# Kernel tuning notes

Hardware: AMD Instinct MI355X
Metric: run time of the kernel (lower is better)

## Reference

```python
import jax, jax.numpy as jnp
import numpy as np

N, DIM, H, DH = 2048, 1024, 16, 64
LARGE_NEG = -1e10
LN_EPS = 1e-6  # flax LayerNorm default


def setup_inputs() -> dict:
    key = jax.random.key(0)
    ks = jax.random.split(key, 6)
    x = jax.random.normal(ks[0], (N, DIM), dtype=jnp.float32)
    pos_sin = jax.random.uniform(ks[1], (N - 1, DH // 2), dtype=jnp.float32)
    pos_cos = jax.random.uniform(ks[2], (N - 1, DH // 2), dtype=jnp.float32)
    mask = jax.random.bernoulli(ks[3], 0.9, (N - 1,))
    ln_scale = jnp.ones((DIM,), jnp.float32)
    ln_bias = jnp.zeros((DIM,), jnp.float32)
    w_qkv = jax.random.normal(ks[4], (DIM, 3 * H * DH), jnp.float32) * (DIM ** -0.5)
    w_out = jax.random.normal(ks[5], (H * DH, DIM), jnp.float32) * ((H * DH) ** -0.5)
    b_out = jnp.zeros((DIM,), jnp.float32)
    return {"x": x, "pos_sin": pos_sin, "pos_cos": pos_cos, "mask": mask,
            "ln_scale": ln_scale, "ln_bias": ln_bias,
            "w_qkv": w_qkv, "w_out": w_out, "b_out": b_out}


def _rotate_every_two(t):
    # t: [i, h, d] -> pairwise rotation along d
    x1 = t[:, :, ::2]
    x2 = t[:, :, 1::2]
    return jnp.stack((-x2, x1), axis=-1).reshape(t.shape)


def _apply_rope(t, sin, cos):
    # sin/cos: [i, d/2] -> interleave-repeat to [i, 1, d] (einops 'b n -> b (n j)', j=2)
    sin2 = jnp.repeat(sin, 2, axis=-1)[:, None, :]
    cos2 = jnp.repeat(cos, 2, axis=-1)[:, None, :]
    return t * cos2 + _rotate_every_two(t) * sin2


def reference(x, pos_sin, pos_cos, mask, ln_scale, ln_bias, w_qkv, w_out, b_out):
    n, dim_in = x.shape
    scale = dim_in ** -0.5  # NOTE: full model dim, as in the source

    # LayerNorm over last axis
    mu = jnp.mean(x, axis=-1, keepdims=True)
    var = jnp.mean(jnp.square(x - mu), axis=-1, keepdims=True)
    xn = (x - mu) * jax.lax.rsqrt(var + LN_EPS) * ln_scale + ln_bias

    # QKV projection (no bias)
    qkv = xn @ w_qkv  # [n, 3*h*d]
    q, k, v = jnp.split(qkv, 3, axis=-1)
    q, k, v = (t.reshape(n, H, DH) for t in (q, k, v))

    # Selective RoPE: rotate all positions except the first token
    q = q.at[1:].set(_apply_rope(q[1:], pos_sin, pos_cos))
    k = k.at[1:].set(_apply_rope(k[1:], pos_sin, pos_cos))

    # Head-last similarity [i, j, h]
    sim = jnp.einsum('ihd,jhd->ijh', q, k) * scale

    # Padding mask: prepend True for position 0, broadcast as (1, j, 1)
    pad_mask = jnp.pad(mask, (1, 0), constant_values=True)[None, :, None]

    # Causal mask: triu of an (n-1)x(n-1) block padded with False on row/col 0
    tri = jnp.pad(jnp.ones((n - 1, n - 1), bool), ((1, 0), (1, 0)), constant_values=False)
    causal_mask = jnp.triu(tri, 1)[:, :, None]  # k = j - i + 1 = 1
    full_mask = (~causal_mask) & pad_mask

    sim = jnp.where(full_mask, sim, LARGE_NEG)
    attn = jax.nn.softmax(sim, axis=-2)  # softmax over j (non-last axis)

    out = jnp.einsum('ijh,jhd->ihd', attn, v).reshape(n, H * DH)
    return out @ w_out + b_out
```

## Files before the change

kernel.cpp:

```cpp
#include <hip/hip_runtime.h>
#include <hip/hip_bf16.h>
#include <stdint.h>

typedef __bf16 bf16_t;
typedef __bf16 bf16x8 __attribute__((ext_vector_type(8)));
typedef __bf16 bf16x4 __attribute__((ext_vector_type(4)));
typedef float  f32x4  __attribute__((ext_vector_type(4)));

#define DEV __device__ __forceinline__

static constexpr int NTOK = 2048;
static constexpr int DIM  = 1024;
static constexpr int NH   = 16;
static constexpr int DH   = 64;
static constexpr int SLOTS_PER_HEAD = 40;
static constexpr int PART_SLOTS = 36;
static constexpr int PART_STRIDE = 17408;
static constexpr float L2E = 1.44269504f;

__device__ static constexpr unsigned char SLOT_ORDER[40] = {
    39, 38, 37, 36, 34, 33, 32, 30, 29, 28, 26, 25, 24, 23,
    22, 21, 19, 18, 16, 15, 13, 12, 11, 10, 8, 6, 4, 3,
    35, 20, 9, 2,
    31, 17, 7, 1,
    27, 14, 5, 0};

DEV void gload_lds16(const void* g, void* l) {
  __builtin_amdgcn_global_load_lds(
      (__attribute__((address_space(1))) void*)(g),
      (__attribute__((address_space(3))) void*)(l), 16, 0, 0);
}

DEV float bf2f(bf16_t b) { return (float)b; }

__global__ __launch_bounds__(256) void k_ln_tc(const float* __restrict__ x,
                                               const float* __restrict__ gamma,
                                               const float* __restrict__ beta,
                                               bf16_t* __restrict__ xn,
                                               const float* __restrict__ wsrc,
                                               bf16_t* __restrict__ wdst,
                                               const float* __restrict__ wosrc,
                                               bf16_t* __restrict__ wodst) {
  __shared__ float tile[64][65];
  __shared__ float red[8];
  int b = blockIdx.x;
  if (b < NTOK) {
    const int row = b;
    const int t = threadIdx.x;
    const float4* x4 = reinterpret_cast<const float4*>(x);
    float4 v = x4[(size_t)row * 256 + t];
    float s  = v.x + v.y + v.z + v.w;
    float s2 = v.x * v.x + v.y * v.y + v.z * v.z + v.w * v.w;
#pragma unroll
    for (int o = 1; o < 64; o <<= 1) {
      s  += __shfl_xor(s, o, 64);
      s2 += __shfl_xor(s2, o, 64);
    }
    const int w = t >> 6, lane = t & 63;
    if (lane == 0) { red[w] = s; red[4 + w] = s2; }
    __syncthreads();
    s  = red[0] + red[1] + red[2] + red[3];
    s2 = red[4] + red[5] + red[6] + red[7];
    const float mu  = s * (1.0f / 1024.0f);
    const float var = s2 * (1.0f / 1024.0f) - mu * mu;
    const float inv = rsqrtf(var + 1e-6f);
    const float4 g = reinterpret_cast<const float4*>(gamma)[t];
    const float4 bb = reinterpret_cast<const float4*>(beta)[t];
    bf16x4 o;
    o[0] = (bf16_t)((v.x - mu) * inv * g.x + bb.x);
    o[1] = (bf16_t)((v.y - mu) * inv * g.y + bb.y);
    o[2] = (bf16_t)((v.z - mu) * inv * g.z + bb.z);
    o[3] = (bf16_t)((v.w - mu) * inv * g.w + bb.w);
    *reinterpret_cast<bf16x4*>(xn + (size_t)row * DIM + t * 4) = o;
  } else if (b < NTOK + 768) {
    b -= NTOK;
    const int c0 = (b % 48) * 64;
    const int r0 = (b / 48) * 64;
    const int tx = threadIdx.x & 63;
    const int ty = threadIdx.x >> 6;
#pragma unroll
    for (int i = 0; i < 16; ++i) {
      int r = ty + i * 4;
      tile[r][tx] = wsrc[(size_t)(r0 + r) * 3072 + c0 + tx];
    }
    __syncthreads();
#pragma unroll
    for (int i = 0; i < 16; ++i) {
      int r = ty + i * 4;
      wdst[(size_t)(c0 + r) * 1024 + r0 + tx] = (bf16_t)tile[tx][r];
    }
  } else {
    b -= (NTOK + 768);
    const int c0 = (b & 15) * 64;
    const int r0 = (b >> 4) * 64;
    const int tx = threadIdx.x & 63;
    const int ty = threadIdx.x >> 6;
#pragma unroll
    for (int i = 0; i < 16; ++i) {
      int r = ty + i * 4;
      tile[r][tx] = wosrc[(size_t)(r0 + r) * 1024 + c0 + tx];
    }
    __syncthreads();
#pragma unroll
    for (int i = 0; i < 16; ++i) {
      int r = ty + i * 4;
      wodst[(size_t)(c0 + r) * 1024 + r0 + tx] = (bf16_t)tile[tx][r];
    }
  }
}

__global__ __launch_bounds__(256) void k_gemm_qkv(const bf16_t* __restrict__ A,
                                                  const bf16_t* __restrict__ Bt,
                                                  bf16_t* __restrict__ Qp,
                                                  bf16_t* __restrict__ Kp,
                                                  bf16_t* __restrict__ Vt,
                                                  const float* __restrict__ psin,
                                                  const float* __restrict__ pcos) {
  __shared__ alignas(16) bf16_t As[2][128 * 32];
  __shared__ alignas(16) bf16_t Bs[2][128 * 32];
  const int K = DIM;
  const int tid = threadIdx.x, lane = tid & 63, w = tid >> 6;
  const int bm = blockIdx.x * 128, bn = blockIdx.y * 128;
  const int wr = (w >> 1) * 64, wc = (w & 1) * 64;
  f32x4 acc[4][4];
#pragma unroll
  for (int i = 0; i < 4; ++i)
#pragma unroll
    for (int j = 0; j < 4; ++j) acc[i][j] = f32x4{0.f, 0.f, 0.f, 0.f};

  const int srow  = lane >> 2;
  const int scol8 = (lane & 3) * 8;

#define GSTAGEQ(KT, BUF)                                                              \
  {                                                                                   \
    _Pragma("unroll") for (int it = 0; it < 2; ++it) {                                \
      int seg = w * 2 + it;                                                           \
      gload_lds16(A  + (size_t)(bm + seg * 16 + srow) * K + (KT) + scol8,             \
                  (char*)As + (BUF) * 8192 + seg * 1024 + lane * 16);                 \
      gload_lds16(Bt + (size_t)(bn + seg * 16 + srow) * K + (KT) + scol8,             \
                  (char*)Bs + (BUF) * 8192 + seg * 1024 + lane * 16);                 \
    }                                                                                 \
  }

  GSTAGEQ(0, 0)
  int buf = 0;
  for (int kt = 0; kt < K; kt += 32, buf ^= 1) {
    if (kt + 32 < K) {
      GSTAGEQ(kt + 32, buf ^ 1)
      asm volatile("s_waitcnt vmcnt(4)" ::: "memory");
    } else {
      asm volatile("s_waitcnt vmcnt(0)" ::: "memory");
    }
    __builtin_amdgcn_s_barrier();
    bf16x8 af[4], bfr[4];
#pragma unroll
    for (int i = 0; i < 4; ++i) {
      int mrow = wr + i * 16 + (lane & 15);
      af[i] = *reinterpret_cast<const bf16x8*>((const char*)As + buf * 8192 + mrow * 64 +
                                               (lane >> 4) * 16);
    }
#pragma unroll
    for (int j = 0; j < 4; ++j) {
      int nrow = wc + j * 16 + (lane & 15);
      bfr[j] = *reinterpret_cast<const bf16x8*>((const char*)Bs + buf * 8192 + nrow * 64 +
                                                (lane >> 4) * 16);
    }
#pragma unroll
    for (int i = 0; i < 4; ++i)
#pragma unroll
      for (int j = 0; j < 4; ++j)
        acc[i][j] = __builtin_amdgcn_mfma_f32_16x16x32_bf16(af[i], bfr[j], acc[i][j], 0, 0, 0);
    __builtin_amdgcn_s_barrier();
  }
#undef GSTAGEQ

  if (bn >= 2048) {
#pragma unroll
    for (int i = 0; i < 4; ++i)
#pragma unroll
      for (int j = 0; j < 4; ++j) {
        int d = bn - 2048 + wc + j * 16 + (lane & 15);
        int n0v = bm + wr + i * 16 + (lane >> 4) * 4;
        bf16x4 v4;
#pragma unroll
        for (int r = 0; r < 4; ++r) v4[r] = (bf16_t)acc[i][j][r];
        *reinterpret_cast<bf16x4*>(Vt + (size_t)d * NTOK + n0v) = v4;
      }
  } else {
#pragma unroll
    for (int i = 0; i < 4; ++i)
#pragma unroll
      for (int j = 0; j < 4; ++j) {
        int nn = bn + wc + j * 16 + (lane & 15);
        int tt = (nn & 63) >> 1;
        bool isq = nn < 1024;
#pragma unroll
        for (int r = 0; r < 4; ++r) {
          int mm = bm + wr + i * 16 + (lane >> 4) * 4 + r;
          float v = acc[i][j][r];
          float p = __shfl_xor(v, 1, 64);
          int pidx = (mm >= 1 ? mm - 1 : 0) * 32 + tt;
          float sn = psin[pidx], cs = pcos[pidx];
          float roped = (nn & 1) ? (v * cs + p * sn) : (v * cs - p * sn);
          if (mm < 1) roped = v;
          if (isq && mm >= 1) roped *= 0.03125f;
          if (isq)
            Qp[(size_t)mm * DIM + nn] = (bf16_t)roped;
          else {
            int hh = (nn - 1024) >> 6, dd = nn & 63;
            Kp[((size_t)hh * NTOK + mm) * DH + dd] = (bf16_t)roped;
          }
        }
      }
  }
}

__global__ __launch_bounds__(256) void k_gemm64(const bf16_t* __restrict__ A,
                                                const bf16_t* __restrict__ Bt,
                                                float* __restrict__ Cf,
                                                const float* __restrict__ bias,
                                                int M, int N, int K) {
  __shared__ alignas(16) bf16_t As[2][64 * 32];
  __shared__ alignas(16) bf16_t Bs[2][64 * 32];
  const int tid = threadIdx.x, lane = tid & 63, w = tid >> 6;
  const int bm = blockIdx.x * 64, bn = blockIdx.y * 64;
  const int wr = (w >> 1) * 32, wc = (w & 1) * 32;
  f32x4 acc[2][2];
#pragma unroll
  for (int i = 0; i < 2; ++i)
#pragma unroll
    for (int j = 0; j < 2; ++j) acc[i][j] = f32x4{0.f, 0.f, 0.f, 0.f};

  const int srow  = lane >> 2;
  const int scol8 = (lane & 3) * 8;

#define GSTAGE64(KT, BUF)                                                             \
  {                                                                                   \
    _Pragma("unroll") for (int it = 0; it < 2; ++it) {                                \
      int s = w * 2 + it;                                                             \
      if (s < 4)                                                                      \
        gload_lds16(A + (size_t)(bm + s * 16 + srow) * K + (KT) + scol8,              \
                    (char*)As + (BUF) * 4096 + s * 1024 + lane * 16);                 \
      else                                                                            \
        gload_lds16(Bt + (size_t)(bn + (s - 4) * 16 + srow) * K + (KT) + scol8,       \
                    (char*)Bs + (BUF) * 4096 + (s - 4) * 1024 + lane * 16);           \
    }                                                                                 \
  }

  GSTAGE64(0, 0)
  int buf = 0;
  for (int kt = 0; kt < K; kt += 32, buf ^= 1) {
    if (kt + 32 < K) {
      GSTAGE64(kt + 32, buf ^ 1)
      asm volatile("s_waitcnt vmcnt(2)" ::: "memory");
    } else {
      asm volatile("s_waitcnt vmcnt(0)" ::: "memory");
    }
    __builtin_amdgcn_s_barrier();
    bf16x8 af[2], bfr[2];
#pragma unroll
    for (int i = 0; i < 2; ++i) {
      int mrow = wr + i * 16 + (lane & 15);
      af[i] = *reinterpret_cast<const bf16x8*>((const char*)As + buf * 4096 + mrow * 64 +
                                               (lane >> 4) * 16);
    }
#pragma unroll
    for (int j = 0; j < 2; ++j) {
      int nrow = wc + j * 16 + (lane & 15);
      bfr[j] = *reinterpret_cast<const bf16x8*>((const char*)Bs + buf * 4096 + nrow * 64 +
                                                (lane >> 4) * 16);
    }
#pragma unroll
    for (int i = 0; i < 2; ++i)
#pragma unroll
      for (int j = 0; j < 2; ++j)
        acc[i][j] = __builtin_amdgcn_mfma_f32_16x16x32_bf16(af[i], bfr[j], acc[i][j], 0, 0, 0);
    __builtin_amdgcn_s_barrier();
  }
#undef GSTAGE64

#pragma unroll
  for (int i = 0; i < 2; ++i)
#pragma unroll
    for (int j = 0; j < 2; ++j)
#pragma unroll
      for (int r = 0; r < 4; ++r) {
        int mm = bm + wr + i * 16 + (lane >> 4) * 4 + r;
        int nn = bn + wc + j * 16 + (lane & 15);
        Cf[(size_t)mm * N + nn] = acc[i][j][r] + bias[nn];
      }
}

__global__ __launch_bounds__(512) void k_attn_part(const bf16_t* __restrict__ Qp,
                                                   const bf16_t* __restrict__ Kp,
                                                   const bf16_t* __restrict__ Vt,
                                                   const int* __restrict__ mask,
                                                   char* __restrict__ part,
                                                   bf16_t* __restrict__ Ob) {
  __shared__ alignas(16) bf16_t Ks[2][64][64];
  __shared__ alignas(16) bf16_t Vs[2][64][64];
  __shared__ alignas(16) float padf[512];

  const int idx = blockIdx.x;
  const int h = idx & 15;
  const int rank = idx >> 4;

  if (rank == 0) {
    float* qv   = padf;
    float* sbuf = (float*)Ks;
    float* red  = (float*)Vs;
    float* red2 = (float*)Vs + 64;
    const int t = threadIdx.x, lane = t & 63, w8 = t >> 6;
    if (t < 64) qv[t] = (float)Qp[h * DH + t];
    __syncthreads();
    float sm[4];
    float lmax = -1e30f;
#pragma unroll
    for (int p = 0; p < 4; ++p) {
      int j = p * 512 + t;
      const bf16_t* kr = Kp + ((size_t)h * NTOK + j) * DH;
      float s = 0.f;
#pragma unroll
      for (int u = 0; u < 8; ++u) {
        bf16x8 kv8 = *reinterpret_cast<const bf16x8*>(kr + u * 8);
#pragma unroll
        for (int e = 0; e < 8; ++e) s += qv[u * 8 + e] * (float)kv8[e];
      }
      bool padj = (j == 0) || (mask[j - 1] != 0);
      s = padj ? s * 0.03125f : -1e30f;
      sm[p] = s;
      lmax = fmaxf(lmax, s);
    }
#pragma unroll
    for (int o = 1; o < 64; o <<= 1) lmax = fmaxf(lmax, __shfl_xor(lmax, o, 64));
    if (lane == 0) red[w8] = lmax;
    __syncthreads();
    float M = red[0];
#pragma unroll
    for (int i = 1; i < 8; ++i) M = fmaxf(M, red[i]);
    __syncthreads();
    float ls = 0.f;
#pragma unroll
    for (int p = 0; p < 4; ++p) {
      float pe = __expf(sm[p] - M);
      sbuf[p * 512 + t] = pe;
      ls += pe;
    }
#pragma unroll
    for (int o = 1; o < 64; o <<= 1) ls += __shfl_xor(ls, o, 64);
    if (lane == 0) red[w8] = ls;
    __syncthreads();
    float L = red[0];
#pragma unroll
    for (int i = 1; i < 8; ++i) L += red[i];

    const int d = t & 63, qr = t >> 6;
    const bf16_t* vr = Vt + ((size_t)h * DH + d) * NTOK + qr * 256;
    float a = 0.f;
#pragma unroll 8
    for (int u = 0; u < 32; ++u) {
      bf16x8 v8 = *reinterpret_cast<const bf16x8*>(vr + u * 8);
#pragma unroll
      for (int e = 0; e < 8; ++e) a += sbuf[qr * 256 + u * 8 + e] * (float)v8[e];
    }
    red2[qr * 64 + d] = a;
    __syncthreads();
    if (t < 64) {
      float o = 0.f;
#pragma unroll
      for (int i = 0; i < 8; ++i) o += red2[i * 64 + t];
      Ob[h * DH + t] = (bf16_t)(o / L);
    }
    return;
  }

  const int slot = SLOT_ORDER[rank - 1];
  int gq;
  if (slot < 4) gq = 0; else if (slot < 12) gq = 1; else if (slot < 24) gq = 2; else gq = 3;
  const int tt = slot - 2 * gq * (gq + 1);
  const int Q = (gq << 2) + tt / (gq + 1);
  const int c2 = tt - (tt / (gq + 1)) * (gq + 1);
  const int q0 = Q * 128;
  const int kbeg = c2 * 512;
  const int kvlen = (Q + 1) * 128;
  const int klen = min(512, kvlen - kbeg);
  const int ntiles = klen >> 6;
  const int nch = gq + 1;

  const int tid = threadIdx.x, lane = tid & 63, w = tid >> 6;
  const int g = lane >> 4;
  const int c = lane & 15;

  for (int jr = tid; jr < klen; jr += 512) {
    int j = kbeg + jr;
    padf[jr] = (j == 0 || mask[j - 1] != 0) ? 1.f : 0.f;
  }

  const int iw = q0 + w * 16;
  bf16x8 qf[2];
  {
    const bf16_t* qp = Qp + (size_t)(iw + c) * DIM + h * DH + g * 8;
    qf[0] = *reinterpret_cast<const bf16x8*>(qp);
    qf[1] = *reinterpret_cast<const bf16x8*>(qp + 32);
  }
  bf16x8 ones;
#pragma unroll
  for (int e = 0; e < 8; ++e) ones[e] = (bf16_t)1.0f;

  float m_run = -1e30f, m2 = -1e30f;
  f32x4 acc[4], accl;
#pragma unroll
  for (int df = 0; df < 4; ++df) acc[df] = f32x4{0.f, 0.f, 0.f, 0.f};
  accl = f32x4{0.f, 0.f, 0.f, 0.f};

  const int r8 = lane >> 3;

#define STAGE(KB, BUF)                                                                   \
  {                                                                                      \
    _Pragma("unroll") for (int i2 = 0; i2 < 2; ++i2) {                                   \
      int s = w * 2 + i2;                                                                \
      int sw = (lane & 7) ^ r8 ^ ((s & 3) << 1);                                         \
      if (s < 8) {                                                                       \
        int row = s * 8 + r8;                                                            \
        gload_lds16(Kp + ((size_t)h * NTOK + (KB) + row) * DH + sw * 8,                  \
                    (char*)Ks + (BUF)*8192 + s * 1024 + lane * 16);                      \
      } else {                                                                           \
        int row = (s - 8) * 8 + r8;                                                      \
        gload_lds16(Vt + ((size_t)h * DH + row) * NTOK + (KB) + sw * 8,                  \
                    (char*)Vs + (BUF)*8192 + (s - 8) * 1024 + lane * 16);                \
      }                                                                                  \
    }                                                                                    \
  }

  STAGE(kbeg, 0)

  for (int it = 0; it < ntiles; ++it) {
    const int buf = it & 1;
    if (it + 1 < ntiles) {
      STAGE(kbeg + (it + 1) * 64, buf ^ 1)
      asm volatile("s_waitcnt vmcnt(2)" ::: "memory");
    } else {
      asm volatile("s_waitcnt vmcnt(0)" ::: "memory");
    }
    __builtin_amdgcn_s_barrier();

    const int k0 = kbeg + it * 64;
    if (k0 <= iw + 15) {
      const char* KsT = (const char*)Ks + buf * 8192;
      const char* VsT = (const char*)Vs + buf * 8192;

      f32x4 sfr[4];
      __builtin_amdgcn_s_setprio(1);
#pragma unroll
      for (int f = 0; f < 4; ++f) {
        int key7 = ((f & 1) * 4) | (c & 3);
        int key = (f >> 1) * 32 + (c >> 2) * 8 + key7;
        int phi = key7 ^ (((c >> 2) & 3) << 1);
        f32x4 s = f32x4{0.f, 0.f, 0.f, 0.f};
#pragma unroll
        for (int kd = 0; kd < 2; ++kd) {
          bf16x8 kf = *reinterpret_cast<const bf16x8*>(
              KsT + key * 128 + (((kd * 4 + g) ^ phi) << 4));
          s = __builtin_amdgcn_mfma_f32_16x16x32_bf16(kf, qf[kd], s, 0, 0, 0);
        }
        sfr[f] = s;
      }
      __builtin_amdgcn_s_setprio(0);

      float pm = fmaxf(fmaxf(sfr[0][0], sfr[0][1]), fmaxf(sfr[0][2], sfr[0][3]));
#pragma unroll
      for (int f = 1; f < 4; ++f)
        pm = fmaxf(pm, fmaxf(fmaxf(sfr[f][0], sfr[f][1]), fmaxf(sfr[f][2], sfr[f][3])));
      pm = fmaxf(pm, __shfl_xor(pm, 16, 64));
      pm = fmaxf(pm, __shfl_xor(pm, 32, 64));

      if (!__all(pm <= m_run + 8.f)) {
        float mnew = fmaxf(m_run, pm);
        float corr = __builtin_amdgcn_exp2f((m_run - mnew) * L2E);
        m_run = mnew;
        m2 = mnew * L2E;
#pragma unroll
        for (int r = 0; r < 4; ++r) {
          float cr = __shfl(corr, g * 4 + r, 64);
          accl[r] *= cr;
#pragma unroll
          for (int df = 0; df < 4; ++df) acc[df][r] *= cr;
        }
      }

      const bool needC = (k0 + 63 > iw);
      const int qlane = iw + c;
      bf16x8 pa[2];
#pragma unroll
      for (int f = 0; f < 4; ++f) {
        int jb = (k0 - kbeg) + (f >> 1) * 32 + g * 8 + (f & 1) * 4;
        f32x4 pad4 = *reinterpret_cast<const f32x4*>(padf + jb);
#pragma unroll
        for (int r = 0; r < 4; ++r) {
          float pe = __builtin_amdgcn_exp2f(__builtin_fmaf(sfr[f][r], L2E, -m2)) * pad4[r];
          if (needC) pe = (kbeg + jb + r <= qlane) ? pe : 0.f;
          pa[f >> 1][(f & 1) * 4 + r] = (bf16_t)pe;
        }
      }

      __builtin_amdgcn_s_setprio(1);
#pragma unroll
      for (int ks = 0; ks < 2; ++ks) {
        accl = __builtin_amdgcn_mfma_f32_16x16x32_bf16(pa[ks], ones, accl, 0, 0, 0);
#pragma unroll
        for (int df = 0; df < 4; ++df) {
          int d = df * 16 + c;
          int phv = (d & 7) ^ (((d >> 3) & 3) << 1);
          bf16x8 vf = *reinterpret_cast<const bf16x8*>(
              VsT + d * 128 + (((ks * 4 + g) ^ phv) << 4));
          acc[df] = __builtin_amdgcn_mfma_f32_16x16x32_bf16(pa[ks], vf, acc[df], 0, 0, 0);
        }
      }
      __builtin_amdgcn_s_setprio(0);
    }
    __builtin_amdgcn_s_barrier();
  }
#undef STAGE

  if (nch == 1) {
#pragma unroll
    for (int r = 0; r < 4; ++r) {
      float inv = 1.0f / accl[r];
      int row = w * 16 + g * 4 + r;
#pragma unroll
      for (int df = 0; df < 4; ++df) {
        if (q0 + row != 0)
          Ob[(size_t)(q0 + row) * DIM + h * DH + df * 16 + c] = (bf16_t)(acc[df][r] * inv);
      }
    }
    return;
  }

  char* pb = part + (size_t)(h * PART_SLOTS + (slot - 4)) * PART_STRIDE;
  bf16_t* po = (bf16_t*)pb;
  float* pmo = (float*)(pb + 16384);
  float* plo = (float*)(pb + 16896);
  float mq[4];
#pragma unroll
  for (int r = 0; r < 4; ++r) mq[r] = __shfl(m2, g * 4 + r, 64);
#pragma unroll
  for (int df = 0; df < 4; ++df)
#pragma unroll
    for (int r = 0; r < 4; ++r) {
      int row = w * 16 + g * 4 + r;
      po[row * 64 + df * 16 + c] = (bf16_t)acc[df][r];
    }
  if (c == 0) {
#pragma unroll
    for (int r = 0; r < 4; ++r) {
      int row = w * 16 + g * 4 + r;
      pmo[row] = mq[r];
      plo[row] = accl[r];
    }
  }
}

__global__ __launch_bounds__(256) void k_merge(const char* __restrict__ part,
                                               bf16_t* __restrict__ Ob) {
  const int Q = blockIdx.x + 4, h = blockIdx.y;
  const int g = Q >> 2, nch = g + 1;
  const int cum = 2 * g * (g + 1) + (Q & 3) * nch - 4;
  const int t = threadIdx.x;
  const int row = t >> 1, half = t & 1;

  float acc[32];
#pragma unroll
  for (int e = 0; e < 32; ++e) acc[e] = 0.f;
  float M = -3e38f, L = 0.f;

  for (int c = 0; c < nch; ++c) {
    const char* pb = part + (size_t)(h * PART_SLOTS + cum + c) * PART_STRIDE;
    float mc = ((const float*)(pb + 16384))[row];
    float lc = ((const float*)(pb + 16896))[row];
    float Mn = fmaxf(M, mc);
    float sOld = __builtin_amdgcn_exp2f(M - Mn), sNew = __builtin_amdgcn_exp2f(mc - Mn);
    M = Mn;
    L = L * sOld + lc * sNew;
    const bf16_t* od = (const bf16_t*)pb + row * 64 + half * 32;
#pragma unroll
    for (int e4 = 0; e4 < 4; ++e4) {
      bf16x8 o8 = *reinterpret_cast<const bf16x8*>(od + e4 * 8);
#pragma unroll
      for (int e = 0; e < 8; ++e)
        acc[e4 * 8 + e] = acc[e4 * 8 + e] * sOld + (float)o8[e] * sNew;
    }
  }
  const float inv = 1.0f / L;
  bf16_t* dst = Ob + (size_t)(Q * 128 + row) * DIM + h * DH + half * 32;
#pragma unroll
  for (int e4 = 0; e4 < 4; ++e4) {
    bf16x8 r8o;
#pragma unroll
    for (int e = 0; e < 8; ++e) r8o[e] = (bf16_t)(acc[e4 * 8 + e] * inv);
    *reinterpret_cast<bf16x8*>(dst + e4 * 8) = r8o;
  }
}

extern "C" void kernel_launch(void* const* d_in, const int* in_sizes, int n_in,
                              void* d_out, int out_size, void* d_ws, size_t ws_size,
                              hipStream_t stream) {
  const float* x       = (const float*)d_in[0];
  const float* pos_sin = (const float*)d_in[1];
  const float* pos_cos = (const float*)d_in[2];
  const int*   mask    = (const int*)d_in[3];
  const float* ln_s    = (const float*)d_in[4];
  const float* ln_b    = (const float*)d_in[5];
  const float* w_qkv   = (const float*)d_in[6];
  const float* w_out   = (const float*)d_in[7];
  const float* b_out   = (const float*)d_in[8];
  float* out = (float*)d_out;

  if (ws_size < 33554432u) return;

  char* ws = (char*)d_ws;
  bf16_t* Qp   = (bf16_t*)(ws + 0);
  bf16_t* Kp   = (bf16_t*)(ws + 4194304);
  bf16_t* Vt   = (bf16_t*)(ws + 8388608);
  bf16_t* Ob   = (bf16_t*)(ws + 12582912);
  bf16_t* Wot  = (bf16_t*)(ws + 16777216);
  bf16_t* xn   = (bf16_t*)(ws + 18874368);
  bf16_t* Wqt  = (bf16_t*)(ws + 23068672);
  char*   part = ws + 18874368;

  k_ln_tc<<<NTOK + 768 + 256, 256, 0, stream>>>(x, ln_s, ln_b, xn, w_qkv, Wqt, w_out, Wot);
  k_gemm_qkv<<<dim3(16, 24), 256, 0, stream>>>(xn, Wqt, Qp, Kp, Vt, pos_sin, pos_cos);
  k_attn_part<<<16 * (SLOTS_PER_HEAD + 1), 512, 0, stream>>>(Qp, Kp, Vt, mask, part, Ob);
  k_merge<<<dim3(12, 16), 256, 0, stream>>>(part, Ob);
  k_gemm64<<<dim3(32, 16), 256, 0, stream>>>(Ob, Wot, out, b_out, NTOK, DIM, DIM);
}
```

Measured before the change: 86.33 us.

## Fuse split-KV merge into attention kernel via last-block atomic counter

Removes the separate merge kernel launch. Each attention partial block atomically increments a per-(head, query-block) counter after writing its partial output, and the last block to arrive combines all partials and writes the normalized result. The counters are zeroed by an extra block in the layernorm/transpose kernel and stored in the output buffer, which the final GEMM later overwrites. This saves a launch and the gap between kernels, at the cost of threadfences, an atomic per block and a serialized merge tail in whichever block finishes last.

```diff
diff --git a/kernel.cpp b/kernel.cpp
--- a/kernel.cpp
+++ b/kernel.cpp
@@ -40,7 +40,8 @@
                                                const float* __restrict__ wsrc,
                                                bf16_t* __restrict__ wdst,
                                                const float* __restrict__ wosrc,
-                                               bf16_t* __restrict__ wodst) {
+                                               bf16_t* __restrict__ wodst,
+                                               int* __restrict__ cnt) {
   __shared__ float tile[64][65];
   __shared__ float red[8];
   int b = blockIdx.x;
@@ -89,7 +90,7 @@
       int r = ty + i * 4;
       wdst[(size_t)(c0 + r) * 1024 + r0 + tx] = (bf16_t)tile[tx][r];
     }
-  } else {
+  } else if (b < NTOK + 768 + 256) {
     b -= (NTOK + 768);
     const int c0 = (b & 15) * 64;
     const int r0 = (b >> 4) * 64;
@@ -106,6 +107,8 @@
       int r = ty + i * 4;
       wodst[(size_t)(c0 + r) * 1024 + r0 + tx] = (bf16_t)tile[tx][r];
     }
+  } else {
+    cnt[threadIdx.x] = 0;
   }
 }
 
@@ -296,10 +299,12 @@
                                                    const bf16_t* __restrict__ Vt,
                                                    const int* __restrict__ mask,
                                                    char* __restrict__ part,
-                                                   bf16_t* __restrict__ Ob) {
+                                                   bf16_t* __restrict__ Ob,
+                                                   int* __restrict__ cnt) {
   __shared__ alignas(16) bf16_t Ks[2][64][64];
   __shared__ alignas(16) bf16_t Vs[2][64][64];
   __shared__ alignas(16) float padf[512];
+  __shared__ int isLast;
 
   const int idx = blockIdx.x;
   const int h = idx & 15;
@@ -537,67 +542,71 @@
   }
 
   char* pb = part + (size_t)(h * PART_SLOTS + (slot - 4)) * PART_STRIDE;
-  bf16_t* po = (bf16_t*)pb;
-  float* pmo = (float*)(pb + 16384);
-  float* plo = (float*)(pb + 16896);
-  float mq[4];
-#pragma unroll
-  for (int r = 0; r < 4; ++r) mq[r] = __shfl(m2, g * 4 + r, 64);
-#pragma unroll
-  for (int df = 0; df < 4; ++df)
-#pragma unroll
-    for (int r = 0; r < 4; ++r) {
-      int row = w * 16 + g * 4 + r;
-      po[row * 64 + df * 16 + c] = (bf16_t)acc[df][r];
-    }
-  if (c == 0) {
-#pragma unroll
-    for (int r = 0; r < 4; ++r) {
-      int row = w * 16 + g * 4 + r;
-      pmo[row] = mq[r];
-      plo[row] = accl[r];
-    }
-  }
-}
-
-__global__ __launch_bounds__(256) void k_merge(const char* __restrict__ part,
-                                               bf16_t* __restrict__ Ob) {
-  const int Q = blockIdx.x + 4, h = blockIdx.y;
-  const int g = Q >> 2, nch = g + 1;
-  const int cum = 2 * g * (g + 1) + (Q & 3) * nch - 4;
-  const int t = threadIdx.x;
-  const int row = t >> 1, half = t & 1;
-
-  float acc[32];
-#pragma unroll
-  for (int e = 0; e < 32; ++e) acc[e] = 0.f;
+  {
+    bf16_t* po = (bf16_t*)pb;
+    float* pmo = (float*)(pb + 16384);
+    float* plo = (float*)(pb + 16896);
+    float mq[4];
+#pragma unroll
+    for (int r = 0; r < 4; ++r) mq[r] = __shfl(m2, g * 4 + r, 64);
+#pragma unroll
+    for (int df = 0; df < 4; ++df)
+#pragma unroll
+      for (int r = 0; r < 4; ++r) {
+        int row = w * 16 + g * 4 + r;
+        po[row * 64 + df * 16 + c] = (bf16_t)acc[df][r];
+      }
+    if (c == 0) {
+#pragma unroll
+      for (int r = 0; r < 4; ++r) {
+        int row = w * 16 + g * 4 + r;
+        pmo[row] = mq[r];
+        plo[row] = accl[r];
+      }
+    }
+  }
+
+  __threadfence();
+  __syncthreads();
+  if (tid == 0) {
+    int old = atomicAdd(&cnt[h * 16 + Q], 1);
+    isLast = (old == nch - 1);
+  }
+  __syncthreads();
+  if (!isLast) return;
+  __threadfence();
+
+  const int cum = 2 * gq * (gq + 1) + (Q & 3) * nch - 4;
+  const int row = tid >> 2, qq = tid & 3;
+  float a2[16];
+#pragma unroll
+  for (int e = 0; e < 16; ++e) a2[e] = 0.f;
   float M = -3e38f, L = 0.f;
-
-  for (int c = 0; c < nch; ++c) {
-    const char* pb = part + (size_t)(h * PART_SLOTS + cum + c) * PART_STRIDE;
-    float mc = ((const float*)(pb + 16384))[row];
-    float lc = ((const float*)(pb + 16896))[row];
+  for (int cc = 0; cc < nch; ++cc) {
+    const char* pc = part + (size_t)(h * PART_SLOTS + cum + cc) * PART_STRIDE;
+    float mc = ((const float*)(pc + 16384))[row];
+    float lc = ((const float*)(pc + 16896))[row];
     float Mn = fmaxf(M, mc);
     float sOld = __builtin_amdgcn_exp2f(M - Mn), sNew = __builtin_amdgcn_exp2f(mc - Mn);
     M = Mn;
     L = L * sOld + lc * sNew;
-    const bf16_t* od = (const bf16_t*)pb + row * 64 + half * 32;
-#pragma unroll
-    for (int e4 = 0; e4 < 4; ++e4) {
-      bf16x8 o8 = *reinterpret_cast<const bf16x8*>(od + e4 * 8);
+    const bf16_t* od = (const bf16_t*)pc + row * 64 + qq * 16;
+#pragma unroll
+    for (int e8 = 0; e8 < 2; ++e8) {
+      bf16x8 o8 = *reinterpret_cast<const bf16x8*>(od + e8 * 8);
 #pragma unroll
       for (int e = 0; e < 8; ++e)
-        acc[e4 * 8 + e] = acc[e4 * 8 + e] * sOld + (float)o8[e] * sNew;
+        a2[e8 * 8 + e] = a2[e8 * 8 + e] * sOld + (float)o8[e] * sNew;
     }
   }
   const float inv = 1.0f / L;
-  bf16_t* dst = Ob + (size_t)(Q * 128 + row) * DIM + h * DH + half * 32;
-#pragma unroll
-  for (int e4 = 0; e4 < 4; ++e4) {
+  bf16_t* dst = Ob + (size_t)(Q * 128 + row) * DIM + h * DH + qq * 16;
+#pragma unroll
+  for (int e8 = 0; e8 < 2; ++e8) {
     bf16x8 r8o;
 #pragma unroll
-    for (int e = 0; e < 8; ++e) r8o[e] = (bf16_t)(acc[e4 * 8 + e] * inv);
-    *reinterpret_cast<bf16x8*>(dst + e4 * 8) = r8o;
+    for (int e = 0; e < 8; ++e) r8o[e] = (bf16_t)(a2[e8 * 8 + e] * inv);
+    *reinterpret_cast<bf16x8*>(dst + e8 * 8) = r8o;
   }
 }
 
@@ -614,6 +623,7 @@
   const float* w_out   = (const float*)d_in[7];
   const float* b_out   = (const float*)d_in[8];
   float* out = (float*)d_out;
+  int* cnt = (int*)d_out;
 
   if (ws_size < 33554432u) return;
 
@@ -627,9 +637,10 @@
   bf16_t* Wqt  = (bf16_t*)(ws + 23068672);
   char*   part = ws + 18874368;
 
-  k_ln_tc<<<NTOK + 768 + 256, 256, 0, stream>>>(x, ln_s, ln_b, xn, w_qkv, Wqt, w_out, Wot);
+  k_ln_tc<<<NTOK + 768 + 256 + 1, 256, 0, stream>>>(x, ln_s, ln_b, xn, w_qkv, Wqt,
+                                                    w_out, Wot, cnt);
   k_gemm_qkv<<<dim3(16, 24), 256, 0, stream>>>(xn, Wqt, Qp, Kp, Vt, pos_sin, pos_cos);
-  k_attn_part<<<16 * (SLOTS_PER_HEAD + 1), 512, 0, stream>>>(Qp, Kp, Vt, mask, part, Ob);
-  k_merge<<<dim3(12, 16), 256, 0, stream>>>(part, Ob);
+  k_attn_part<<<16 * (SLOTS_PER_HEAD + 1), 512, 0, stream>>>(Qp, Kp, Vt, mask, part, Ob,
+                                                             cnt);
   k_gemm64<<<dim3(32, 16), 256, 0, stream>>>(Ob, Wot, out, b_out, NTOK, DIM, DIM);
 }
```

Result: slower. 273.0 us (+216.2%).
